# Kernel tuning notes

Hardware: AMD Instinct MI355X
Metric: run time of the kernel (lower is better)

Reference implementation:

```python
import jax, jax.numpy as jnp
import numpy as np

B, S, D, K = 2048, 200, 64, 4  # batch, seq_len, dim, num_interest


def setup_inputs() -> dict:
    key = jax.random.key(0)
    k1, k2, k3, k4 = jax.random.split(key, 4)
    item_his_emb = jax.random.normal(k1, (B, S, D), dtype=jnp.float32)
    item_eb = jax.random.normal(k2, (B, D), dtype=jnp.float32)
    mask = jax.random.randint(k3, (B, S), 0, 2, dtype=jnp.int32)
    W = jax.random.normal(k4, (D, K * D), dtype=jnp.float32) * 0.05
    b = jnp.zeros((K * D,), dtype=jnp.float32)
    return {"item_his_emb": item_his_emb, "item_eb": item_eb, "mask": mask, "W": W, "b": b}


def _squash(v):
    # v: [B, K, D]; squash nonlinearity with the module's epsilon
    n2 = jnp.sum(jnp.square(v), axis=-1, keepdims=True)
    return (n2 / (1.0 + n2) / jnp.sqrt(n2 + 1e-9)) * v


def reference(item_his_emb, item_eb, mask, W, b):
    # bilinear_type == 1: Dense(dim * num_interest)
    hat = item_his_emb @ W + b                      # [B, S, K*D]
    hat = hat.reshape(B, S, K, D).transpose(0, 2, 1, 3)  # [B, K, S, D]

    mask_zero = (mask == 0)[:, None, :]             # [B, 1, S] broadcast over K
    cw = jnp.zeros((B, K, S), dtype=item_his_emb.dtype)

    interest = None
    for i in range(3):
        sw = jax.nn.softmax(cw, axis=1)             # softmax over interests
        sw = jnp.where(mask_zero, 0.0, sw)          # [B, K, S]
        interest = _squash(jnp.einsum('bks,bksd->bkd', sw, hat))  # [B, K, D]
        if i < 2:
            cw = cw + jnp.einsum('bksd,bkd->bks', hat, interest)

    # readout: softmax attention over interests against target item, hard argmax gather
    atten = jax.nn.softmax(jnp.einsum('bkd,bd->bk', interest, item_eb), axis=1)
    idx = jnp.argmax(atten, axis=1)                 # [B]
    readout = jnp.take_along_axis(interest, idx[:, None, None], axis=1)[:, 0, :]  # [B, D]
    return interest, readout
```

## Files before the change

kernel.cpp:

```cpp
#include <hip/hip_runtime.h>


#define NB 2048
#define NS 200
#define ND 64
#define NK 4
#define NT 512
#define LOG2E 1.44269504f

__device__ __forceinline__ int rot(int s) { return (s + (s >> 3)) & 15; }

__device__ __forceinline__ void gload16(const float* g_, float* l_) {
  __builtin_amdgcn_global_load_lds(
      (const __attribute__((address_space(1))) unsigned int*)g_,
      (__attribute__((address_space(3))) unsigned int*)l_, 16, 0, 0);
}

template <int CTRL>
__device__ __forceinline__ float dppadd(float v) {
  int p = __builtin_amdgcn_update_dpp(0, __float_as_int(v), CTRL, 0xF, 0xF, true);
  return v + __int_as_float(p);
}

#if __has_builtin(__builtin_amdgcn_permlane16_swap)
__device__ __forceinline__ float pl16add(float v) {
  auto r = __builtin_amdgcn_permlane16_swap(__float_as_int(v), __float_as_int(v),
                                            false, false);
  return __int_as_float(r[0]) + __int_as_float(r[1]);
}
#else
__device__ __forceinline__ float pl16add(float v) { return v + __shfl_xor(v, 16, 64); }
#endif

#if __has_builtin(__builtin_amdgcn_permlane32_swap)
__device__ __forceinline__ float pl32add(float v) {
  auto r = __builtin_amdgcn_permlane32_swap(__float_as_int(v), __float_as_int(v),
                                            false, false);
  return __int_as_float(r[0]) + __int_as_float(r[1]);
}
#else
__device__ __forceinline__ float pl32add(float v) { return v + __shfl_xor(v, 32, 64); }
#endif

__device__ __forceinline__ float red_j(float v) {
  v = dppadd<0x124>(v);
  v = dppadd<0x128>(v);
  v = pl16add(v);
  v = pl32add(v);
  return v;
}
__device__ __forceinline__ float red_q(float v) {
  v = dppadd<0xB1>(v);
  v = dppadd<0x4E>(v);
  return v;
}
__device__ __forceinline__ float red64(float v) { return red_j(red_q(v)); }

__global__ __launch_bounds__(NT, 2) void caps_kernel(
    const float* __restrict__ his, const float* __restrict__ itemeb,
    const int* __restrict__ mask, const float* __restrict__ W,
    const float* __restrict__ bias, float* __restrict__ out) {
  __shared__ float semb[NS * ND];
  __shared__ float pe[8][NK][ND];
  __shared__ float sG[NK][ND];
  __shared__ float su[NK][ND];
  __shared__ float spv[NK][ND];
  __shared__ float smsk[NS];
  __shared__ float4 pts4[8];
  __shared__ __align__(16) float soff[NK];
  __shared__ float satt[NK];
  __shared__ int sidx;

  const int t = threadIdx.x;
  const int w = t >> 6, l = t & 63;
  const int g = l & 3, j = l >> 2;
  const int gid = (w << 2) | g;
  const int ke = w & 3, h_ = w >> 2;
  const int b = blockIdx.x;
  const float* eb = his + (size_t)b * NS * ND;

  float wreg[32];
#pragma unroll
  for (int c = 0; c < 32; ++c)
    wreg[c] = W[(size_t)(32 * h_ + c) * (NK * ND) + ke * ND + l];
  float breg = bias[ke * ND + l];
  float iq = itemeb[(size_t)b * ND + l];

  {
    const int sg = l >> 4, sj = l & 15;
    for (int i = w; i < 50; i += 8) {
      int s = 4 * i + sg;
      int q = (sj - rot(s)) & 15;
      gload16(eb + (s << 6) + (q << 2), &semb[i * 256]);
    }
  }
  if (t < NS) smsk[t] = (mask[(size_t)b * NS + t] != 0) ? 1.0f : 0.0f;
  __syncthreads();

  const int ntr = (w < 2) ? 7 : 6;
  float greg = 0.f;

  for (int it = 0; it < 3; ++it) {
    float4 a0 = {0, 0, 0, 0}, a1 = {0, 0, 0, 0}, a2 = {0, 0, 0, 0},
           a3 = {0, 0, 0, 0};
    float t0 = 0, t1 = 0, t2 = 0, t3 = 0;

    if (it == 0) {
      for (int tt = 0; tt < ntr; ++tt) {
        int s = gid + 32 * tt;
        float4 eq = *(const float4*)&semb[(s << 6) + 4 * ((j + rot(s)) & 15)];
        float sw = 0.25f * smsk[s];
        a0.x += sw * eq.x; a0.y += sw * eq.y;
        a0.z += sw * eq.z; a0.w += sw * eq.w;
        t0 += sw;
      }
      a0.x = red_q(a0.x); a0.y = red_q(a0.y);
      a0.z = red_q(a0.z); a0.w = red_q(a0.w);
      t0 = red_q(t0);
      a1 = a0; a2 = a0; a3 = a0; t1 = t0; t2 = t0; t3 = t0;
    } else {
      float4 u0 = *(const float4*)&su[0][4 * j];
      float4 u1 = *(const float4*)&su[1][4 * j];
      float4 u2 = *(const float4*)&su[2][4 * j];
      float4 u3 = *(const float4*)&su[3][4 * j];
      float4 sof = *(const float4*)&soff[0];
      for (int tt = 0; tt < ntr; ++tt) {
        int s = gid + 32 * tt;
        float4 eq = *(const float4*)&semb[(s << 6) + 4 * ((j + rot(s)) & 15)];
        float mk = smsk[s];
        float lg0 = eq.x * u0.x + eq.y * u0.y + eq.z * u0.z + eq.w * u0.w;
        float lg1 = eq.x * u1.x + eq.y * u1.y + eq.z * u1.z + eq.w * u1.w;
        float lg2 = eq.x * u2.x + eq.y * u2.y + eq.z * u2.z + eq.w * u2.w;
        float lg3 = eq.x * u3.x + eq.y * u3.y + eq.z * u3.z + eq.w * u3.w;
        lg0 = red_j(lg0) + sof.x;
        lg1 = red_j(lg1) + sof.y;
        lg2 = red_j(lg2) + sof.z;
        lg3 = red_j(lg3) + sof.w;
        float e0 = exp2f(lg0), e1 = exp2f(lg1);
        float e2 = exp2f(lg2), e3 = exp2f(lg3);
        float r = mk / (e0 + e1 + e2 + e3);
        float sw0 = e0 * r, sw1 = e1 * r, sw2 = e2 * r, sw3 = e3 * r;
        a0.x += sw0 * eq.x; a0.y += sw0 * eq.y; a0.z += sw0 * eq.z; a0.w += sw0 * eq.w;
        a1.x += sw1 * eq.x; a1.y += sw1 * eq.y; a1.z += sw1 * eq.z; a1.w += sw1 * eq.w;
        a2.x += sw2 * eq.x; a2.y += sw2 * eq.y; a2.z += sw2 * eq.z; a2.w += sw2 * eq.w;
        a3.x += sw3 * eq.x; a3.y += sw3 * eq.y; a3.z += sw3 * eq.z; a3.w += sw3 * eq.w;
        t0 += sw0; t1 += sw1; t2 += sw2; t3 += sw3;
      }
      a0.x = red_q(a0.x); a0.y = red_q(a0.y); a0.z = red_q(a0.z); a0.w = red_q(a0.w);
      a1.x = red_q(a1.x); a1.y = red_q(a1.y); a1.z = red_q(a1.z); a1.w = red_q(a1.w);
      a2.x = red_q(a2.x); a2.y = red_q(a2.y); a2.z = red_q(a2.z); a2.w = red_q(a2.w);
      a3.x = red_q(a3.x); a3.y = red_q(a3.y); a3.z = red_q(a3.z); a3.w = red_q(a3.w);
      t0 = red_q(t0); t1 = red_q(t1); t2 = red_q(t2); t3 = red_q(t3);
    }
    if (g == 0) {
      *(float4*)&pe[w][0][4 * j] = a0;
      *(float4*)&pe[w][1][4 * j] = a1;
      *(float4*)&pe[w][2][4 * j] = a2;
      *(float4*)&pe[w][3][4 * j] = a3;
    }
    if (l == 0) pts4[w] = make_float4(t0, t1, t2, t3);
    __syncthreads();

    {
      int cl = 32 * h_ + (l & 31);
      float sse = 0.f;
#pragma unroll
      for (int w2 = 0; w2 < 8; ++w2) sse += pe[w2][ke][cl];
      su[ke][cl] = sse;
      float vp = 0.f;
#pragma unroll
      for (int q2 = 0; q2 < 8; ++q2) {
        float4 e4 = *(const float4*)&su[ke][32 * h_ + 4 * q2];
        vp += e4.x * wreg[4 * q2 + 0] + e4.y * wreg[4 * q2 + 1] +
              e4.z * wreg[4 * q2 + 2] + e4.w * wreg[4 * q2 + 3];
      }
      if (h_) spv[ke][l] = vp;
      __syncthreads();

      if (h_ == 0) {
        float ts_ = 0.f;
#pragma unroll
        for (int w2 = 0; w2 < 8; ++w2) ts_ += ((const float*)&pts4[w2])[ke];
        float accv = vp + spv[ke][l] + ts_ * breg;
        float n2 = red64(accv * accv);
        float scale = n2 / (1.f + n2) / sqrtf(n2 + 1e-9f);
        float inter = scale * accv;
        if (it < 2) {
          greg += inter;
          sG[ke][l] = greg;
          float ob = red64(breg * greg);
          if (l == 0) soff[ke] = ob * LOG2E;
          const float4* Wr =
              (const float4*)(W + (size_t)l * (NK * ND) + ke * ND);
          const float4* Gk = (const float4*)&sG[ke][0];
          float a = 0.f;
#pragma unroll
          for (int d4 = 0; d4 < 16; ++d4) {
            float4 wv = Wr[d4], gv = Gk[d4];
            a += wv.x * gv.x + wv.y * gv.y + wv.z * gv.z + wv.w * gv.w;
          }
          su[ke][l] = LOG2E * a;
        } else {
          out[((size_t)b * NK + ke) * ND + l] = inter;
          float dot_ = red64(inter * iq);
          spv[ke][l] = inter;
          if (l == 0) satt[ke] = dot_;
        }
      }
      __syncthreads();
    }
  }

  if (t == 0) {
    int bi = 0;
    float bv = satt[0];
#pragma unroll
    for (int kk = 1; kk < NK; ++kk)
      if (satt[kk] > bv) { bv = satt[kk]; bi = kk; }
    sidx = bi;
  }
  __syncthreads();
  if (t < ND) out[(size_t)NB * NK * ND + (size_t)b * ND + t] = spv[sidx][t];
}

extern "C" void kernel_launch(void* const* d_in, const int* in_sizes, int n_in,
                              void* d_out, int out_size, void* d_ws, size_t ws_size,
                              hipStream_t stream) {
  (void)in_sizes; (void)n_in; (void)out_size; (void)d_ws; (void)ws_size;
  const float* his = (const float*)d_in[0];
  const float* itemeb = (const float*)d_in[1];
  const int* mask = (const int*)d_in[2];
  const float* W = (const float*)d_in[3];
  const float* bias = (const float*)d_in[4];
  float* out = (float*)d_out;
  caps_kernel<<<NB, NT, 0, stream>>>(his, itemeb, mask, W, bias, out);
}
```

Baseline: 91.14 us.

## Collapse split-half projection into four waves to drop a barrier per iteration

```diff
diff --git a/kernel.cpp b/kernel.cpp
--- a/kernel.cpp
+++ b/kernel.cpp
@@ -75,14 +75,16 @@
   const int w = t >> 6, l = t & 63;
   const int g = l & 3, j = l >> 2;
   const int gid = (w << 2) | g;
-  const int ke = w & 3, h_ = w >> 2;
+  const int ke = w & 3;
   const int b = blockIdx.x;
   const float* eb = his + (size_t)b * NS * ND;
 
-  float wreg[32];
-#pragma unroll
-  for (int c = 0; c < 32; ++c)
-    wreg[c] = W[(size_t)(32 * h_ + c) * (NK * ND) + ke * ND + l];
+  float wreg[64];
+  if (w < 4) {
+#pragma unroll
+    for (int c = 0; c < 64; ++c)
+      wreg[c] = W[(size_t)c * (NK * ND) + ke * ND + l];
+  }
   float breg = bias[ke * ND + l];
   float iq = itemeb[(size_t)b * ND + l];
 
@@ -117,7 +119,6 @@
       a0.x = red_q(a0.x); a0.y = red_q(a0.y);
       a0.z = red_q(a0.z); a0.w = red_q(a0.w);
       t0 = red_q(t0);
-      a1 = a0; a2 = a0; a3 = a0; t1 = t0; t2 = t0; t3 = t0;
     } else {
       float4 u0 = *(const float4*)&su[0][4 * j];
       float4 u1 = *(const float4*)&su[1][4 * j];
@@ -154,61 +155,56 @@
     }
     if (g == 0) {
       *(float4*)&pe[w][0][4 * j] = a0;
-      *(float4*)&pe[w][1][4 * j] = a1;
-      *(float4*)&pe[w][2][4 * j] = a2;
-      *(float4*)&pe[w][3][4 * j] = a3;
+      if (it > 0) {
+        *(float4*)&pe[w][1][4 * j] = a1;
+        *(float4*)&pe[w][2][4 * j] = a2;
+        *(float4*)&pe[w][3][4 * j] = a3;
+      }
     }
     if (l == 0) pts4[w] = make_float4(t0, t1, t2, t3);
     __syncthreads();
 
-    {
-      int cl = 32 * h_ + (l & 31);
+    if (w < 4) {
+      const int kk = (it == 0) ? 0 : ke;
       float sse = 0.f;
 #pragma unroll
-      for (int w2 = 0; w2 < 8; ++w2) sse += pe[w2][ke][cl];
-      su[ke][cl] = sse;
-      float vp = 0.f;
-#pragma unroll
-      for (int q2 = 0; q2 < 8; ++q2) {
-        float4 e4 = *(const float4*)&su[ke][32 * h_ + 4 * q2];
-        vp += e4.x * wreg[4 * q2 + 0] + e4.y * wreg[4 * q2 + 1] +
-              e4.z * wreg[4 * q2 + 2] + e4.w * wreg[4 * q2 + 3];
-      }
-      if (h_) spv[ke][l] = vp;
-      __syncthreads();
-
-      if (h_ == 0) {
-        float ts_ = 0.f;
-#pragma unroll
-        for (int w2 = 0; w2 < 8; ++w2) ts_ += ((const float*)&pts4[w2])[ke];
-        float accv = vp + spv[ke][l] + ts_ * breg;
-        float n2 = red64(accv * accv);
-        float scale = n2 / (1.f + n2) / sqrtf(n2 + 1e-9f);
-        float inter = scale * accv;
-        if (it < 2) {
-          greg += inter;
-          sG[ke][l] = greg;
-          float ob = red64(breg * greg);
-          if (l == 0) soff[ke] = ob * LOG2E;
-          const float4* Wr =
-              (const float4*)(W + (size_t)l * (NK * ND) + ke * ND);
-          const float4* Gk = (const float4*)&sG[ke][0];
-          float a = 0.f;
-#pragma unroll
-          for (int d4 = 0; d4 < 16; ++d4) {
-            float4 wv = Wr[d4], gv = Gk[d4];
-            a += wv.x * gv.x + wv.y * gv.y + wv.z * gv.z + wv.w * gv.w;
-          }
-          su[ke][l] = LOG2E * a;
-        } else {
-          out[((size_t)b * NK + ke) * ND + l] = inter;
-          float dot_ = red64(inter * iq);
-          spv[ke][l] = inter;
-          if (l == 0) satt[ke] = dot_;
+      for (int w2 = 0; w2 < 8; ++w2) sse += pe[w2][kk][l];
+      su[ke][l] = sse;
+      float ts_ = 0.f;
+#pragma unroll
+      for (int w2 = 0; w2 < 8; ++w2) ts_ += ((const float*)&pts4[w2])[kk];
+      float accv = ts_ * breg;
+#pragma unroll
+      for (int q2 = 0; q2 < 16; ++q2) {
+        float4 e4 = *(const float4*)&su[ke][4 * q2];
+        accv += e4.x * wreg[4 * q2 + 0] + e4.y * wreg[4 * q2 + 1] +
+                e4.z * wreg[4 * q2 + 2] + e4.w * wreg[4 * q2 + 3];
+      }
+      float n2 = red64(accv * accv);
+      float scale = n2 / (1.f + n2) / sqrtf(n2 + 1e-9f);
+      float inter = scale * accv;
+      if (it < 2) {
+        greg += inter;
+        sG[ke][l] = greg;
+        float ob = red64(breg * greg);
+        if (l == 0) soff[ke] = ob * LOG2E;
+        const float4* Wr = (const float4*)(W + (size_t)l * (NK * ND) + ke * ND);
+        const float4* Gk = (const float4*)&sG[ke][0];
+        float a = 0.f;
+#pragma unroll
+        for (int d4 = 0; d4 < 16; ++d4) {
+          float4 wv = Wr[d4], gv = Gk[d4];
+          a += wv.x * gv.x + wv.y * gv.y + wv.z * gv.z + wv.w * gv.w;
         }
-      }
-      __syncthreads();
-    }
+        su[ke][l] = LOG2E * a;
+      } else {
+        out[((size_t)b * NK + ke) * ND + l] = inter;
+        float dot_ = red64(inter * iq);
+        spv[ke][l] = inter;
+        if (l == 0) satt[ke] = dot_;
+      }
+    }
+    __syncthreads();
   }
 
   if (t == 0) {
```

Result: slower. 127.2 us (+39.5%).
